# Kernel tuning notes

Measured on AMD Instinct MI355X. Metric: run time of the kernel, lower is better.

The kernel has to match this reference:

```python
import jax, jax.numpy as jnp
import numpy as np

NEG_INF = -1000000000.0

def setup_inputs() -> dict:
    key = jax.random.key(0)
    k1, k2, k3, k4 = jax.random.split(key, 4)
    N, F_in, F_out, H = 4096, 256, 64, 4
    x = jax.random.normal(k1, (N, F_in), dtype=jnp.float32)
    adj = jax.random.randint(k2, (N, N), 0, 2, dtype=jnp.int32)
    W = jax.random.normal(k3, (H, F_in, F_out), dtype=jnp.float32) * 0.05
    a = jax.random.normal(k4, (H, 2 * F_out, 1), dtype=jnp.float32) * 0.05
    return {"x": x, "adj": adj, "W": W, "a": a}

def reference(x, adj, W, a):
    # x: [N, F_in], adj: [N, N] int, W: [H, F_in, F_out], a: [H, 2*F_out, 1]
    H, F_in, F_out = W.shape
    N = x.shape[0]
    h = jnp.einsum('nf,hfo->hno', x, W)              # [H, N, F_out]
    a1 = a[:, :F_out, 0]                             # [H, F_out] (dot with h_i part of concat)
    a2 = a[:, F_out:, 0]                             # [H, F_out] (dot with h_j part)
    f1 = jnp.einsum('hno,ho->hn', h, a1)             # [H, N]
    f2 = jnp.einsum('hno,ho->hn', h, a2)             # [H, N]
    e = f1[:, :, None] + f2[:, None, :]              # [H, N, N] == dot(concat(h_i,h_j), a)
    e = jnp.where(e >= 0, e, 0.2 * e)                # leaky_relu, slope 0.2
    mask = (adj == 0).astype(jnp.float32) * NEG_INF  # [N, N]
    alpha = jax.nn.softmax(e + mask[None], axis=-1)  # [H, N, N]
    # dropout deterministic (training=False) -> identity
    out = jnp.einsum('hij,hjo->hio', alpha, h)       # [H, N, F_out]
    # concat=True: concat heads along feature dim
    return jnp.transpose(out, (1, 0, 2)).reshape(N, H * F_out)
```

## Files before the change

kernel.cpp:

```cpp
#include <hip/hip_runtime.h>
#include <hip/hip_bf16.h>
#include <stdint.h>

#define LOG2E  1.4426950408889634f
#define LOG2E5 0.28853900817779268f

typedef __attribute__((ext_vector_type(4))) float f4;
typedef __attribute__((ext_vector_type(4))) int   i4;
typedef __attribute__((ext_vector_type(8))) short s8;
typedef __attribute__((ext_vector_type(4))) short s4;

#if defined(__has_builtin)
# if __has_builtin(__builtin_amdgcn_exp2f)
#  define EXP2F(x) __builtin_amdgcn_exp2f(x)
# else
#  define EXP2F(x) exp2f(x)
# endif
#else
# define EXP2F(x) exp2f(x)
#endif

static __device__ __forceinline__ uint32_t fbits(float f) {
  union { float f; uint32_t u; } c; c.f = f; return c.u;
}
static __device__ __forceinline__ float ubits(uint32_t u) {
  union { uint32_t u; float f; } c; c.u = u; return c.f;
}
static __device__ __forceinline__ uint16_t bf16_rne(float f) {
  uint32_t b = fbits(f);
  b += 0x7FFFu + ((b >> 16) & 1u);
  return (uint16_t)(b >> 16);
}
static __device__ __forceinline__ uint32_t fkey(float f) {
  uint32_t u = fbits(f);
  return (u >> 31) ? ~u : (u | 0x80000000u);
}
static __device__ __forceinline__ float unkey(uint32_t k) {
  return ubits((k & 0x80000000u) ? (k ^ 0x80000000u) : ~k);
}

__global__ __launch_bounds__(256) void k_pack_prep(
    const int* __restrict__ adj, uint32_t* __restrict__ bitsR,
    const float* __restrict__ W, uint16_t* __restrict__ WT,
    uint32_t* __restrict__ f2mkey) {
  int b = blockIdx.x;
  if (b < 2048) {
    int id = b * 256 + threadIdx.x;
    const int* src = adj + ((size_t)id << 5);
    i4 v[8];
    #pragma unroll
    for (int m = 0; m < 8; ++m) v[m] = *(const i4*)(src + (m << 2));
    uint32_t w = 0;
    #pragma unroll
    for (int m = 0; m < 8; ++m) {
      w |= ((uint32_t)v[m].x) << (4 * m);
      w |= ((uint32_t)v[m].y) << (4 * m + 1);
      w |= ((uint32_t)v[m].z) << (4 * m + 2);
      w |= ((uint32_t)v[m].w) << (4 * m + 3);
    }
    bitsR[id] = w;
  } else {
    int bb = b - 2048;
    if (bb == 0 && threadIdx.x < 4) f2mkey[threadIdx.x] = 0u;
    int idx = (bb * 256 + threadIdx.x) * 4;
    f4 w = *(const f4*)(W + idx);
    int h = idx >> 14;
    int k = (idx >> 6) & 255;
    int o = idx & 63;
    uint16_t* base = WT + ((h << 6) + o) * 256 + k;
    base[0]   = bf16_rne(w.x);
    base[256] = bf16_rne(w.y);
    base[512] = bf16_rne(w.z);
    base[768] = bf16_rne(w.w);
  }
}

__global__ __launch_bounds__(256) void k_gemm_h(
    const float* __restrict__ x, const uint16_t* __restrict__ WT,
    const float* __restrict__ a,
    uint16_t* __restrict__ hTf, float* __restrict__ f1, float* __restrict__ f2,
    uint32_t* __restrict__ f2mkey) {
  const int N = 4096, K = 256;
  __shared__ uint16_t xs[16][264];
  int t = threadIdx.x;
  int i0 = blockIdx.x * 16;
  {
    int r = t >> 4, c = (t & 15) << 4;
    const float* src = x + (i0 + r) * K + c;
    union { uint16_t u[16]; s8 v[2]; } tmp;
    #pragma unroll
    for (int i = 0; i < 16; i += 4) {
      f4 v = *(const f4*)(src + i);
      tmp.u[i+0] = bf16_rne(v.x); tmp.u[i+1] = bf16_rne(v.y);
      tmp.u[i+2] = bf16_rne(v.z); tmp.u[i+3] = bf16_rne(v.w);
    }
    *(s8*)&xs[r][c]     = tmp.v[0];
    *(s8*)&xs[r][c + 8] = tmp.v[1];
  }
  __syncthreads();
  int wave = t >> 6, lane = t & 63, lr = lane & 15, lc = lane >> 4;
  f4 acc[4];
  #pragma unroll
  for (int cg = 0; cg < 4; ++cg) acc[cg] = (f4){0.f, 0.f, 0.f, 0.f};
  #pragma unroll
  for (int ks = 0; ks < 8; ++ks) {
    s8 af = *(const s8*)&xs[lr][ks * 32 + lc * 8];
    #pragma unroll
    for (int cg = 0; cg < 4; ++cg) {
      s8 bf = *(const s8*)(WT + ((wave << 6) + (cg << 4) + lr) * 256 + ks * 32 + lc * 8);
      acc[cg] = __builtin_amdgcn_mfma_f32_16x16x32_bf16(af, bf, acc[cg], 0, 0, 0);
    }
  }
  float p1[4] = {0, 0, 0, 0}, p2[4] = {0, 0, 0, 0};
  #pragma unroll
  for (int cg = 0; cg < 4; ++cg) {
    float a1v = a[wave * 128 + (cg << 4) + lr];
    float a2v = a[wave * 128 + 64 + (cg << 4) + lr];
    #pragma unroll
    for (int q = 0; q < 4; ++q) {
      p1[q] = fmaf(acc[cg][q], a1v, p1[q]);
      p2[q] = fmaf(acc[cg][q], a2v, p2[q]);
    }
  }
  #pragma unroll
  for (int m = 1; m <= 8; m <<= 1) {
    #pragma unroll
    for (int q = 0; q < 4; ++q) {
      p1[q] += __shfl_xor(p1[q], m, 64);
      p2[q] += __shfl_xor(p2[q], m, 64);
    }
  }
  if (lr == 0) {
    #pragma unroll
    for (int q = 0; q < 4; ++q) {
      f1[wave * N + i0 + (lc << 2) + q] = p1[q];
      f2[wave * N + i0 + (lc << 2) + q] = p2[q];
    }
  }
  float wm = fmaxf(fmaxf(p2[0], p2[1]), fmaxf(p2[2], p2[3]));
  wm = fmaxf(wm, __shfl_xor(wm, 16, 64));
  wm = fmaxf(wm, __shfl_xor(wm, 32, 64));
  if (lane == 0) atomicMax(&f2mkey[wave], fkey(wm));
  int b0 = (i0 & 31) + (lc << 2);
  int hi = b0 >> 3, e0 = b0 & 7;
  size_t cbase = ((size_t)(wave * 32 + (i0 >> 7)) * 4 + ((i0 >> 5) & 3)) << 2;
  #pragma unroll
  for (int cg = 0; cg < 4; ++cg) {
    union { uint16_t u[4]; s4 v; } h4;
    #pragma unroll
    for (int q = 0; q < 4; ++q) h4.u[q] = bf16_rne(acc[cg][q]);
    *(s4*)(hTf + ((cbase + cg) << 9) + ((hi << 4) + lr) * 8 + e0) = h4.v;
  }
}

__global__ __launch_bounds__(256, 4) void k_attn(
    const uint32_t* __restrict__ bitsR, const float* __restrict__ f1,
    const float* __restrict__ f2, const uint32_t* __restrict__ f2mkey,
    const uint16_t* __restrict__ hTf, float* __restrict__ out) {
  const int N = 4096;
  __shared__ uint32_t lb[16][132];
  __shared__ float Ored[4][64][18];
  __shared__ float lred[4][16];
  int h = blockIdx.x & 3, rb = blockIdx.x >> 2;
  int R0 = rb << 4;
  int t = threadIdx.x, wq = t >> 6, lane = t & 63, lr = lane & 15, lc = lane >> 4;

  {
    int r = t >> 4, w8 = (t & 15) << 3;
    const uint32_t* src = bitsR + ((size_t)(R0 + r) << 7) + w8;
    i4 v0 = *(const i4*)src;
    i4 v1 = *(const i4*)(src + 4);
    *(i4*)&lb[r][w8]     = v0;
    *(i4*)&lb[r][w8 + 4] = v1;
  }

  float fm = unkey(f2mkey[h]);
  float f1v = f1[h * N + R0 + lr];
  float s = f1v + fm;
  float M = fmaxf(s, 0.2f * s);
  float d1 = fmaf(f1v, LOG2E, -M * LOG2E);
  float d2 = fmaf(f1v, LOG2E5, -M * LOG2E);

  f4 acc[4], accl = {0.f, 0.f, 0.f, 0.f};
  #pragma unroll
  for (int cg = 0; cg < 4; ++cg) acc[cg] = (f4){0.f, 0.f, 0.f, 0.f};
  const s8 ones = {0x3F80, 0x3F80, 0x3F80, 0x3F80, 0x3F80, 0x3F80, 0x3F80, 0x3F80};

  const float* fb = f2 + h * N + (wq << 10) + (lc << 3);
  const uint16_t* hbase = hTf + (((size_t)(h * 512) + (wq << 7)) << 9) + lane * 8;
  int sh = lc << 3;

  __syncthreads();

  f4 cf0 = *(const f4*)(fb), cf1 = *(const f4*)(fb + 4);
  s8 cb0 = *(const s8*)(hbase);
  s8 cb1 = *(const s8*)(hbase + 512);
  s8 cb2 = *(const s8*)(hbase + 1024);
  s8 cb3 = *(const s8*)(hbase + 1536);

  for (int c = 0; c < 32; ++c) {
    f4 nf0 = cf0, nf1 = cf1;
    s8 nb0 = cb0, nb1 = cb1, nb2 = cb2, nb3 = cb3;
    if (c + 1 < 32) {
      nf0 = *(const f4*)(fb + ((c + 1) << 5));
      nf1 = *(const f4*)(fb + ((c + 1) << 5) + 4);
      const uint16_t* hc = hbase + ((size_t)(c + 1) << 11);
      nb0 = *(const s8*)(hc);
      nb1 = *(const s8*)(hc + 512);
      nb2 = *(const s8*)(hc + 1024);
      nb3 = *(const s8*)(hc + 1536);
    }
    uint32_t ws = lb[lr][(wq << 5) + c] >> sh;
    uint32_t eb[8];
    #pragma unroll
    for (int e = 0; e < 8; ++e) {
      float f2e = (e < 4) ? cf0[e] : cf1[e - 4];
      float arg = fmaxf(fmaf(f2e, LOG2E, d1),
                        fmaf(f2e, LOG2E5, d2));
      uint32_t msk = 0u - ((ws >> e) & 1u);
      eb[e] = (fbits(EXP2F(arg)) & msk) + 0x8000u;
    }
    union { uint32_t u[4]; s8 v; } af;
    #pragma unroll
    for (int i2 = 0; i2 < 4; ++i2)
      af.u[i2] = __builtin_amdgcn_perm(eb[2 * i2 + 1], eb[2 * i2], 0x07060302u);
    acc[0] = __builtin_amdgcn_mfma_f32_16x16x32_bf16(af.v, cb0, acc[0], 0, 0, 0);
    acc[1] = __builtin_amdgcn_mfma_f32_16x16x32_bf16(af.v, cb1, acc[1], 0, 0, 0);
    acc[2] = __builtin_amdgcn_mfma_f32_16x16x32_bf16(af.v, cb2, acc[2], 0, 0, 0);
    acc[3] = __builtin_amdgcn_mfma_f32_16x16x32_bf16(af.v, cb3, acc[3], 0, 0, 0);
    accl   = __builtin_amdgcn_mfma_f32_16x16x32_bf16(af.v, ones, accl, 0, 0, 0);
    cf0 = nf0; cf1 = nf1;
    cb0 = nb0; cb1 = nb1; cb2 = nb2; cb3 = nb3;
  }

  #pragma unroll
  for (int cg = 0; cg < 4; ++cg)
    *(f4*)&Ored[wq][(cg << 4) + lr][lc << 2] = acc[cg];
  if (lr == 0) *(f4*)&lred[wq][lc << 2] = accl;
  __syncthreads();

  int o = t >> 2, ig = (t & 3) << 2;
  f4 sum = {0.f, 0.f, 0.f, 0.f}, lsf = {0.f, 0.f, 0.f, 0.f};
  #pragma unroll
  for (int w = 0; w < 4; ++w) {
    sum += *(const f4*)&Ored[w][o][ig];
    lsf += *(const f4*)&lred[w][ig];
  }
  #pragma unroll
  for (int k = 0; k < 4; ++k) {
    float l = lsf[k];
    float r = sum[k] * ((l > 0.f) ? 1.0f / l : 0.f);
    out[(size_t)(R0 + ig + k) * 256 + (h << 6) + o] = r;
  }
}

extern "C" void kernel_launch(void* const* d_in, const int* in_sizes, int n_in,
                              void* d_out, int out_size, void* d_ws, size_t ws_size,
                              hipStream_t stream) {
  (void)in_sizes; (void)n_in; (void)out_size; (void)ws_size;
  const float* x   = (const float*)d_in[0];
  const int*   adj = (const int*)d_in[1];
  const float* W   = (const float*)d_in[2];
  const float* a   = (const float*)d_in[3];
  float* out = (float*)d_out;
  char* ws = (char*)d_ws;

  size_t oWT = 0;
  size_t oHT = oWT + 131072;
  size_t oF1 = oHT + 2097152;
  size_t oF2 = oF1 + 65536;
  size_t oFM = oF2 + 65536;
  size_t oBT = (oFM + 16 + 255) & ~(size_t)255;

  uint16_t* WT    = (uint16_t*)(ws + oWT);
  uint16_t* hTf   = (uint16_t*)(ws + oHT);
  float*    f1    = (float*)(ws + oF1);
  float*    f2    = (float*)(ws + oF2);
  uint32_t* f2mk  = (uint32_t*)(ws + oFM);
  uint32_t* bitsR = (uint32_t*)(ws + oBT);

  k_pack_prep<<<2112, 256, 0, stream>>>(adj, bitsR, W, WT, f2mk);
  k_gemm_h<<<256, 256, 0, stream>>>(x, WT, a, hTf, f1, f2, f2mk);
  k_attn<<<1024, 256, 0, stream>>>(bitsR, f1, f2, f2mk, hTf, out);
}
```

Baseline: 63.08 us.

## Double attention row tile per block and merge adj packing into GEMM kernel

The attention kernel now processes 32 rows per block instead of 16, so each loaded hT/f2 chunk feeds two row groups of MFMAs. Its inner loop is restructured into a double-buffered 64-column step. The adjacency bit-packing moves out of the weight-prep kernel and into the GEMM kernel's grid, so packing runs alongside the h projection, and the small W transpose gets its own launch. The intent is to halve the hT/f2 global traffic per output and overlap the adj packing with the GEMM. In exchange, register pressure rises (launch bounds drop to 2 blocks per CU) and only 512 attention blocks are launched, which may reduce occupancy.

```diff
diff --git a/kernel.cpp b/kernel.cpp
--- a/kernel.cpp
+++ b/kernel.cpp
@@ -39,13 +39,33 @@
   return ubits((k & 0x80000000u) ? (k ^ 0x80000000u) : ~k);
 }
 
-__global__ __launch_bounds__(256) void k_pack_prep(
-    const int* __restrict__ adj, uint32_t* __restrict__ bitsR,
-    const float* __restrict__ W, uint16_t* __restrict__ WT,
-    uint32_t* __restrict__ f2mkey) {
-  int b = blockIdx.x;
-  if (b < 2048) {
-    int id = b * 256 + threadIdx.x;
+__global__ __launch_bounds__(256) void k_prep(const float* __restrict__ W,
+                                              uint16_t* __restrict__ WT,
+                                              uint32_t* __restrict__ f2mkey) {
+  if (blockIdx.x == 0 && threadIdx.x < 4) f2mkey[threadIdx.x] = 0u;
+  int idx = (blockIdx.x * 256 + threadIdx.x) * 4;
+  f4 w = *(const f4*)(W + idx);
+  int h = idx >> 14;
+  int k = (idx >> 6) & 255;
+  int o = idx & 63;
+  uint16_t* base = WT + ((h << 6) + o) * 256 + k;
+  base[0]   = bf16_rne(w.x);
+  base[256] = bf16_rne(w.y);
+  base[512] = bf16_rne(w.z);
+  base[768] = bf16_rne(w.w);
+}
+
+__global__ __launch_bounds__(256) void k_work(
+    const float* __restrict__ x, const uint16_t* __restrict__ WT,
+    const float* __restrict__ a,
+    uint16_t* __restrict__ hTf, float* __restrict__ f1, float* __restrict__ f2,
+    uint32_t* __restrict__ f2mkey,
+    const int* __restrict__ adj, uint32_t* __restrict__ bitsR) {
+  const int N = 4096, K = 256;
+  __shared__ uint16_t xs[16][264];
+  int b = blockIdx.x, t = threadIdx.x;
+  if (b >= 256) {
+    int id = (b - 256) * 256 + t;
     const int* src = adj + ((size_t)id << 5);
     i4 v[8];
     #pragma unroll
@@ -59,31 +79,9 @@
       w |= ((uint32_t)v[m].w) << (4 * m + 3);
     }
     bitsR[id] = w;
-  } else {
-    int bb = b - 2048;
-    if (bb == 0 && threadIdx.x < 4) f2mkey[threadIdx.x] = 0u;
-    int idx = (bb * 256 + threadIdx.x) * 4;
-    f4 w = *(const f4*)(W + idx);
-    int h = idx >> 14;
-    int k = (idx >> 6) & 255;
-    int o = idx & 63;
-    uint16_t* base = WT + ((h << 6) + o) * 256 + k;
-    base[0]   = bf16_rne(w.x);
-    base[256] = bf16_rne(w.y);
-    base[512] = bf16_rne(w.z);
-    base[768] = bf16_rne(w.w);
-  }
-}
-
-__global__ __launch_bounds__(256) void k_gemm_h(
-    const float* __restrict__ x, const uint16_t* __restrict__ WT,
-    const float* __restrict__ a,
-    uint16_t* __restrict__ hTf, float* __restrict__ f1, float* __restrict__ f2,
-    uint32_t* __restrict__ f2mkey) {
-  const int N = 4096, K = 256;
-  __shared__ uint16_t xs[16][264];
-  int t = threadIdx.x;
-  int i0 = blockIdx.x * 16;
+    return;
+  }
+  int i0 = b << 4;
   {
     int r = t >> 4, c = (t & 15) << 4;
     const float* src = x + (i0 + r) * K + c;
@@ -153,37 +151,43 @@
   }
 }
 
-__global__ __launch_bounds__(256, 4) void k_attn(
+__global__ __launch_bounds__(256, 2) void k_attn(
     const uint32_t* __restrict__ bitsR, const float* __restrict__ f1,
     const float* __restrict__ f2, const uint32_t* __restrict__ f2mkey,
     const uint16_t* __restrict__ hTf, float* __restrict__ out) {
   const int N = 4096;
-  __shared__ uint32_t lb[16][132];
-  __shared__ float Ored[4][64][18];
-  __shared__ float lred[4][16];
+  __shared__ uint32_t lb[32][132];
+  __shared__ float Ored[4][64][35];
+  __shared__ float lred[4][32];
   int h = blockIdx.x & 3, rb = blockIdx.x >> 2;
-  int R0 = rb << 4;
+  int R0 = rb << 5;
   int t = threadIdx.x, wq = t >> 6, lane = t & 63, lr = lane & 15, lc = lane >> 4;
 
   {
-    int r = t >> 4, w8 = (t & 15) << 3;
-    const uint32_t* src = bitsR + ((size_t)(R0 + r) << 7) + w8;
-    i4 v0 = *(const i4*)src;
-    i4 v1 = *(const i4*)(src + 4);
-    *(i4*)&lb[r][w8]     = v0;
-    *(i4*)&lb[r][w8 + 4] = v1;
+    int r = t >> 3, wb = (t & 7) << 4;
+    const uint32_t* src = bitsR + ((size_t)(R0 + r) << 7) + wb;
+    #pragma unroll
+    for (int m = 0; m < 4; ++m)
+      *(i4*)&lb[r][wb + (m << 2)] = *(const i4*)(src + (m << 2));
   }
 
   float fm = unkey(f2mkey[h]);
-  float f1v = f1[h * N + R0 + lr];
-  float s = f1v + fm;
-  float M = fmaxf(s, 0.2f * s);
-  float d1 = fmaf(f1v, LOG2E, -M * LOG2E);
-  float d2 = fmaf(f1v, LOG2E5, -M * LOG2E);
-
-  f4 acc[4], accl = {0.f, 0.f, 0.f, 0.f};
-  #pragma unroll
-  for (int cg = 0; cg < 4; ++cg) acc[cg] = (f4){0.f, 0.f, 0.f, 0.f};
+  float d1[2], d2[2];
+  #pragma unroll
+  for (int g = 0; g < 2; ++g) {
+    float f1v = f1[h * N + R0 + (g << 4) + lr];
+    float s = f1v + fm;
+    float M = fmaxf(s, 0.2f * s);
+    d1[g] = fmaf(f1v, LOG2E, -M * LOG2E);
+    d2[g] = fmaf(f1v, LOG2E5, -M * LOG2E);
+  }
+  f4 acc[2][4], accl[2];
+  #pragma unroll
+  for (int g = 0; g < 2; ++g) {
+    accl[g] = (f4){0.f, 0.f, 0.f, 0.f};
+    #pragma unroll
+    for (int cg = 0; cg < 4; ++cg) acc[g][cg] = (f4){0.f, 0.f, 0.f, 0.f};
+  }
   const s8 ones = {0x3F80, 0x3F80, 0x3F80, 0x3F80, 0x3F80, 0x3F80, 0x3F80, 0x3F80};
 
   const float* fb = f2 + h * N + (wq << 10) + (lc << 3);
@@ -192,65 +196,86 @@
 
   __syncthreads();
 
-  f4 cf0 = *(const f4*)(fb), cf1 = *(const f4*)(fb + 4);
-  s8 cb0 = *(const s8*)(hbase);
-  s8 cb1 = *(const s8*)(hbase + 512);
-  s8 cb2 = *(const s8*)(hbase + 1024);
-  s8 cb3 = *(const s8*)(hbase + 1536);
-
-  for (int c = 0; c < 32; ++c) {
-    f4 nf0 = cf0, nf1 = cf1;
-    s8 nb0 = cb0, nb1 = cb1, nb2 = cb2, nb3 = cb3;
-    if (c + 1 < 32) {
-      nf0 = *(const f4*)(fb + ((c + 1) << 5));
-      nf1 = *(const f4*)(fb + ((c + 1) << 5) + 4);
-      const uint16_t* hc = hbase + ((size_t)(c + 1) << 11);
-      nb0 = *(const s8*)(hc);
-      nb1 = *(const s8*)(hc + 512);
-      nb2 = *(const s8*)(hc + 1024);
-      nb3 = *(const s8*)(hc + 1536);
-    }
-    uint32_t ws = lb[lr][(wq << 5) + c] >> sh;
-    uint32_t eb[8];
-    #pragma unroll
-    for (int e = 0; e < 8; ++e) {
-      float f2e = (e < 4) ? cf0[e] : cf1[e - 4];
-      float arg = fmaxf(fmaf(f2e, LOG2E, d1),
-                        fmaf(f2e, LOG2E5, d2));
-      uint32_t msk = 0u - ((ws >> e) & 1u);
-      eb[e] = (fbits(EXP2F(arg)) & msk) + 0x8000u;
-    }
-    union { uint32_t u[4]; s8 v; } af;
-    #pragma unroll
-    for (int i2 = 0; i2 < 4; ++i2)
-      af.u[i2] = __builtin_amdgcn_perm(eb[2 * i2 + 1], eb[2 * i2], 0x07060302u);
-    acc[0] = __builtin_amdgcn_mfma_f32_16x16x32_bf16(af.v, cb0, acc[0], 0, 0, 0);
-    acc[1] = __builtin_amdgcn_mfma_f32_16x16x32_bf16(af.v, cb1, acc[1], 0, 0, 0);
-    acc[2] = __builtin_amdgcn_mfma_f32_16x16x32_bf16(af.v, cb2, acc[2], 0, 0, 0);
-    acc[3] = __builtin_amdgcn_mfma_f32_16x16x32_bf16(af.v, cb3, acc[3], 0, 0, 0);
-    accl   = __builtin_amdgcn_mfma_f32_16x16x32_bf16(af.v, ones, accl, 0, 0, 0);
-    cf0 = nf0; cf1 = nf1;
-    cb0 = nb0; cb1 = nb1; cb2 = nb2; cb3 = nb3;
-  }
-
-  #pragma unroll
-  for (int cg = 0; cg < 4; ++cg)
-    *(f4*)&Ored[wq][(cg << 4) + lr][lc << 2] = acc[cg];
-  if (lr == 0) *(f4*)&lred[wq][lc << 2] = accl;
+  f4 cfA[4], cfB[4];
+  s8 cbA[8], cbB[8];
+
+#define LOADC(C, CF, CB)                                                    \
+  {                                                                         \
+    const float* fp_ = fb + ((C) << 6);                                     \
+    CF[0] = *(const f4*)fp_;        CF[1] = *(const f4*)(fp_ + 4);          \
+    CF[2] = *(const f4*)(fp_ + 32); CF[3] = *(const f4*)(fp_ + 36);         \
+    const uint16_t* hp_ = hbase + ((size_t)(C) << 12);                      \
+    CB[0] = *(const s8*)(hp_);        CB[1] = *(const s8*)(hp_ + 512);      \
+    CB[2] = *(const s8*)(hp_ + 1024); CB[3] = *(const s8*)(hp_ + 1536);     \
+    CB[4] = *(const s8*)(hp_ + 2048); CB[5] = *(const s8*)(hp_ + 2560);     \
+    CB[6] = *(const s8*)(hp_ + 3072); CB[7] = *(const s8*)(hp_ + 3584);     \
+  }
+
+#define COMPUTE(C, CF, CB)                                                  \
+  {                                                                         \
+    _Pragma("unroll")                                                       \
+    for (int g = 0; g < 2; ++g) {                                           \
+      int row_ = (g << 4) + lr;                                             \
+      int w0_ = (wq << 5) + ((C) << 1);                                     \
+      uint32_t wsa_ = lb[row_][w0_] >> sh;                                  \
+      uint32_t wsb_ = lb[row_][w0_ + 1] >> sh;                              \
+      _Pragma("unroll")                                                     \
+      for (int ks = 0; ks < 2; ++ks) {                                      \
+        uint32_t ws_ = ks ? wsb_ : wsa_;                                    \
+        uint32_t eb_[8];                                                    \
+        _Pragma("unroll")                                                   \
+        for (int e = 0; e < 8; ++e) {                                       \
+          float f2e_ = CF[(ks << 1) + (e >> 2)][e & 3];                     \
+          float arg_ = fmaxf(fmaf(f2e_, LOG2E, d1[g]),                      \
+                             fmaf(f2e_, LOG2E5, d2[g]));                    \
+          uint32_t msk_ = 0u - ((ws_ >> e) & 1u);                           \
+          eb_[e] = (fbits(EXP2F(arg_)) & msk_) + 0x8000u;                   \
+        }                                                                   \
+        union { uint32_t u[4]; s8 v; } af_;                                 \
+        _Pragma("unroll")                                                   \
+        for (int i2 = 0; i2 < 4; ++i2)                                      \
+          af_.u[i2] = __builtin_amdgcn_perm(eb_[2*i2+1], eb_[2*i2],         \
+                                            0x07060302u);                   \
+        acc[g][0] = __builtin_amdgcn_mfma_f32_16x16x32_bf16(af_.v,          \
+                        CB[(ks<<2)],     acc[g][0], 0, 0, 0);               \
+        acc[g][1] = __builtin_amdgcn_mfma_f32_16x16x32_bf16(af_.v,          \
+                        CB[(ks<<2) + 1], acc[g][1], 0, 0, 0);               \
+        acc[g][2] = __builtin_amdgcn_mfma_f32_16x16x32_bf16(af_.v,          \
+                        CB[(ks<<2) + 2], acc[g][2], 0, 0, 0);               \
+        acc[g][3] = __builtin_amdgcn_mfma_f32_16x16x32_bf16(af_.v,          \
+                        CB[(ks<<2) + 3], acc[g][3], 0, 0, 0);               \
+        accl[g]   = __builtin_amdgcn_mfma_f32_16x16x32_bf16(af_.v,          \
+                        ones, accl[g], 0, 0, 0);                            \
+      }                                                                     \
+    }                                                                       \
+  }
+
+  LOADC(0, cfA, cbA);
+  for (int cc = 0; cc < 16; cc += 2) {
+    LOADC(cc + 1, cfB, cbB);
+    COMPUTE(cc, cfA, cbA);
+    if (cc < 14) LOADC(cc + 2, cfA, cbA);
+    COMPUTE(cc + 1, cfB, cbB);
+  }
+#undef LOADC
+#undef COMPUTE
+
+  #pragma unroll
+  for (int g = 0; g < 2; ++g) {
+    #pragma unroll
+    for (int cg = 0; cg < 4; ++cg)
+      *(f4*)&Ored[wq][(cg << 4) + lr][(g << 4) + (lc << 2)] = acc[g][cg];
+    if (lr == 0) *(f4*)&lred[wq][(g << 4) + (lc << 2)] = accl[g];
+  }
   __syncthreads();
 
-  int o = t >> 2, ig = (t & 3) << 2;
-  f4 sum = {0.f, 0.f, 0.f, 0.f}, lsf = {0.f, 0.f, 0.f, 0.f};
-  #pragma unroll
-  for (int w = 0; w < 4; ++w) {
-    sum += *(const f4*)&Ored[w][o][ig];
-    lsf += *(const f4*)&lred[w][ig];
-  }
-  #pragma unroll
-  for (int k = 0; k < 4; ++k) {
-    float l = lsf[k];
-    float r = sum[k] * ((l > 0.f) ? 1.0f / l : 0.f);
-    out[(size_t)(R0 + ig + k) * 256 + (h << 6) + o] = r;
+  int o = t & 63, ib = (t >> 6) << 3;
+  #pragma unroll
+  for (int k = 0; k < 8; ++k) {
+    int i = ib + k;
+    float l = lred[0][i] + lred[1][i] + lred[2][i] + lred[3][i];
+    float sv = Ored[0][o][i] + Ored[1][o][i] + Ored[2][o][i] + Ored[3][o][i];
+    out[(size_t)(R0 + i) * 256 + (h << 6) + o] = sv * ((l > 0.f) ? 1.0f / l : 0.f);
   }
 }
 
@@ -279,7 +304,7 @@
   uint32_t* f2mk  = (uint32_t*)(ws + oFM);
   uint32_t* bitsR = (uint32_t*)(ws + oBT);
 
-  k_pack_prep<<<2112, 256, 0, stream>>>(adj, bitsR, W, WT, f2mk);
-  k_gemm_h<<<256, 256, 0, stream>>>(x, WT, a, hTf, f1, f2, f2mk);
-  k_attn<<<1024, 256, 0, stream>>>(bitsR, f1, f2, f2mk, hTf, out);
-}
+  k_prep<<<64, 256, 0, stream>>>(W, WT, f2mk);
+  k_work<<<2304, 256, 0, stream>>>(x, WT, a, hTf, f1, f2, f2mk, adj, bitsR);
+  k_attn<<<512, 256, 0, stream>>>(bitsR, f1, f2, f2mk, hTf, out);
+}
```

Result: faster. 61.27 us (-2.9%).
